# Performance work log

Measured on AMD Instinct MI355X. Metric: run time of the kernel, lower is better.

Reference implementation:

```python
import jax, jax.numpy as jnp
import numpy as np

N = 100000   # nodes
E = 800000   # edges
D_IN = 96
D_H = 96


def setup_inputs() -> dict:
    key = jax.random.key(0)
    ks = jax.random.split(key, 6)
    s = 1.0 / np.sqrt(D_IN)
    return {
        "x": jax.random.normal(ks[0], (N, D_IN), jnp.float32),
        "edge_index": jax.random.randint(ks[1], (2, E), 0, N, dtype=jnp.int32),
        "W1": jax.random.normal(ks[2], (D_IN, D_H), jnp.float32) * s,
        "b1": jnp.zeros((D_H,), jnp.float32),
        "W2": jax.random.normal(ks[3], (D_H, D_H), jnp.float32) * (1.0 / np.sqrt(D_H)),
        "b2": jnp.zeros((D_H,), jnp.float32),
    }


def _gcn_norm(edge_index, n):
    # add self-loops, then symmetric normalization deg^-1/2 * deg^-1/2 (PyG gcn_norm)
    loop = jnp.arange(n, dtype=edge_index.dtype)
    src = jnp.concatenate([edge_index[0], loop])  # [E+N] message sources
    dst = jnp.concatenate([edge_index[1], loop])  # [E+N] aggregation targets
    deg = jax.ops.segment_sum(jnp.ones_like(dst, jnp.float32), dst, num_segments=n)
    dis = jax.lax.rsqrt(deg)  # deg >= 1 thanks to self-loops
    norm = dis[src] * dis[dst]  # [E+N]
    return src, dst, norm


def _gcn_layer(x, W, b, src, dst, norm, n):
    h = x @ W                                  # [N, D] dense transform
    msg = h[src] * norm[:, None]               # [E+N, D] gather + scale
    agg = jax.ops.segment_sum(msg, dst, num_segments=n)  # scatter-add
    return agg + b


def reference(x, edge_index, W1, b1, W2, b2):
    src, dst, norm = _gcn_norm(edge_index, N)
    h = jax.nn.relu(_gcn_layer(x, W1, b1, src, dst, norm, N))
    z = jax.nn.relu(_gcn_layer(h, W2, b2, src, dst, norm, N))
    return z
```

## Files before the change

### kernel.cpp

```cpp
#include <hip/hip_runtime.h>

#define D 96
#define BSH 9
#define BNODES 512
#define MAXBUK 256


__global__ __launch_bounds__(256) void p1_hist(const int* __restrict__ ei,
                                               int* __restrict__ bcnt, int e) {
    __shared__ int h[MAXBUK];
    for (int i = threadIdx.x; i < MAXBUK; i += 256) h[i] = 0;
    __syncthreads();
    for (int i = blockIdx.x * 256 + threadIdx.x; i < e; i += gridDim.x * 256)
        atomicAdd(&h[ei[e + i] >> BSH], 1);
    __syncthreads();
    for (int i = threadIdx.x; i < MAXBUK; i += 256)
        if (h[i]) atomicAdd(&bcnt[i], h[i]);
}

__global__ void p1_scan(const int* __restrict__ bcnt, int* __restrict__ bbase,
                        int* __restrict__ bcur, int e, int nbuk) {
    __shared__ int s[MAXBUK];
    int t = threadIdx.x;
    int v = (t < nbuk) ? bcnt[t] : 0;
    s[t] = v;
    __syncthreads();
    for (int off = 1; off < MAXBUK; off <<= 1) {
        int u = (t >= off) ? s[t - off] : 0;
        __syncthreads();
        s[t] += u;
        __syncthreads();
    }
    int ex = s[t] - v;
    bbase[t] = ex;
    bcur[t] = ex;
    if (t == MAXBUK - 1) bbase[MAXBUK] = e;
}

__global__ __launch_bounds__(256) void p2_part(const int* __restrict__ ei,
                                               int* __restrict__ bcur,
                                               int2* __restrict__ pairs, int e) {
    __shared__ int h[MAXBUK];
    __shared__ int base[MAXBUK];
    __shared__ int offs[MAXBUK];
    const int CHUNK = 8192;
    int begin = blockIdx.x * CHUNK;
    int endc = min(begin + CHUNK, e);
    for (int i = threadIdx.x; i < MAXBUK; i += 256) h[i] = 0;
    __syncthreads();
    for (int i = begin + threadIdx.x; i < endc; i += 256)
        atomicAdd(&h[ei[e + i] >> BSH], 1);
    __syncthreads();
    for (int i = threadIdx.x; i < MAXBUK; i += 256) {
        int c = h[i];
        base[i] = c ? atomicAdd(&bcur[i], c) : 0;
        offs[i] = 0;
    }
    __syncthreads();
    for (int i = begin + threadIdx.x; i < endc; i += 256) {
        int d = ei[e + i], sv = ei[i];
        int b = d >> BSH;
        int r = atomicAdd(&offs[b], 1);
        pairs[base[b] + r] = make_int2(d, sv);
    }
}

__global__ __launch_bounds__(256) void p3_build(const int2* __restrict__ pairs,
                                                const int* __restrict__ bbase,
                                                int* __restrict__ rp, float* __restrict__ dis,
                                                int* __restrict__ esrc, int n, int e) {
    __shared__ int deg[BNODES];
    __shared__ int cur[BNODES];
    __shared__ int ps[256];
    int b = blockIdx.x;
    int node0 = b << BSH;
    int t = threadIdx.x;
    int pbeg = bbase[b], pend = bbase[b + 1];
    deg[t] = 0; deg[t + 256] = 0;
    __syncthreads();
    for (int i = pbeg + t; i < pend; i += 256)
        atomicAdd(&deg[pairs[i].x - node0], 1);
    __syncthreads();
    int d0 = deg[2 * t], d1 = deg[2 * t + 1];
    int pv = d0 + d1;
    ps[t] = pv;
    __syncthreads();
    for (int off = 1; off < 256; off <<= 1) {
        int u = (t >= off) ? ps[t - off] : 0;
        __syncthreads();
        ps[t] += u;
        __syncthreads();
    }
    int ex = ps[t] - pv;
    int e0 = ex, e1 = ex + d0;
    cur[2 * t] = e0; cur[2 * t + 1] = e1;
    int n0 = node0 + 2 * t, n1 = n0 + 1;
    if (n0 < n) { rp[n0] = pbeg + e0; dis[n0] = rsqrtf((float)(d0 + 1)); }
    if (n1 < n) { rp[n1] = pbeg + e1; dis[n1] = rsqrtf((float)(d1 + 1)); }
    if (b == 0 && t == 0) rp[n] = e;
    __syncthreads();
    for (int i = pbeg + t; i < pend; i += 256) {
        int2 p = pairs[i];
        int r = atomicAdd(&cur[p.x - node0], 1);
        esrc[pbeg + r] = p.y;
    }
}


__global__ void wt_kernel(const float* __restrict__ W1, const float* __restrict__ W2,
                          float* __restrict__ Wt1, float* __restrict__ Wt2) {
    int i = blockIdx.x * 256 + threadIdx.x;
    if (i < D * D) {
        int k = i / D, c = i % D;
        Wt1[c * D + k] = W1[i];
        Wt2[c * D + k] = W2[i];
    }
}


#define KC 32
#define XS_S 36
#define WT_S 36

__global__ __launch_bounds__(256) void gemm_scale(const float* __restrict__ X,
                                                  const float* __restrict__ Wt,
                                                  const float* __restrict__ dis,
                                                  float* __restrict__ out, int n) {
    __shared__ float xs[128 * XS_S];
    __shared__ float wt[96 * WT_S];
    int t = threadIdx.x;
    int row0 = blockIdx.x * 128;
    int rg = t & 15;
    int cg = t >> 4;
    float acc[8][6] = {};

    for (int kc = 0; kc < D; kc += KC) {
        for (int i = t; i < 96 * 8; i += 256) {
            int c = i >> 3, c4 = i & 7;
            float4 v = *(const float4*)&Wt[c * D + kc + c4 * 4];
            *(float4*)&wt[c * WT_S + c4 * 4] = v;
        }
        for (int i = t; i < 128 * 8; i += 256) {
            int r = i >> 3, c4 = i & 7;
            int gr = row0 + r;
            float4 v = (gr < n) ? *(const float4*)&X[(size_t)gr * D + kc + c4 * 4]
                                : make_float4(0.f, 0.f, 0.f, 0.f);
            *(float4*)&xs[r * XS_S + 4 * (c4 ^ ((r >> 3) & 7))] = v;
        }
        __syncthreads();
        #pragma unroll
        for (int k4 = 0; k4 < 8; ++k4) {
            float4 a[8], b[6];
            int xk = 4 * (k4 ^ (rg & 7));
            #pragma unroll
            for (int i = 0; i < 8; ++i)
                a[i] = *(const float4*)&xs[(rg * 8 + i) * XS_S + xk];
            #pragma unroll
            for (int j = 0; j < 6; ++j)
                b[j] = *(const float4*)&wt[(cg * 6 + j) * WT_S + k4 * 4];
            #pragma unroll
            for (int i = 0; i < 8; ++i)
                #pragma unroll
                for (int j = 0; j < 6; ++j) {
                    acc[i][j] += a[i].x * b[j].x;
                    acc[i][j] += a[i].y * b[j].y;
                    acc[i][j] += a[i].z * b[j].z;
                    acc[i][j] += a[i].w * b[j].w;
                }
        }
        __syncthreads();
    }
    #pragma unroll
    for (int i = 0; i < 8; ++i) {
        int gr = row0 + rg * 8 + i;
        if (gr < n) {
            float dsc = dis[gr];
            #pragma unroll
            for (int j = 0; j < 6; ++j)
                out[(size_t)gr * D + cg * 6 + j] = dsc * acc[i][j];
        }
    }
}


__global__ __launch_bounds__(256) void agg_kernel(const float* __restrict__ hs,
                                                  const float* __restrict__ dis,
                                                  const float* __restrict__ bias,
                                                  const int* __restrict__ rp,
                                                  const int* __restrict__ esrc,
                                                  float* __restrict__ out, int n) {
    int lane = threadIdx.x & 31;
    int node = blockIdx.x * 8 + (threadIdx.x >> 5);
    if (node >= n || lane >= 24) return;
    float4 s = ((const float4*)(hs + (size_t)node * D))[lane];
    float4 s2 = make_float4(0.f, 0.f, 0.f, 0.f);
    int beg = rp[node], end = rp[node + 1];
    int e = beg;
    for (; e + 1 < end; e += 2) {
        float4 v0 = ((const float4*)(hs + (size_t)esrc[e] * D))[lane];
        float4 v1 = ((const float4*)(hs + (size_t)esrc[e + 1] * D))[lane];
        s.x += v0.x;  s.y += v0.y;  s.z += v0.z;  s.w += v0.w;
        s2.x += v1.x; s2.y += v1.y; s2.z += v1.z; s2.w += v1.w;
    }
    if (e < end) {
        float4 v0 = ((const float4*)(hs + (size_t)esrc[e] * D))[lane];
        s.x += v0.x; s.y += v0.y; s.z += v0.z; s.w += v0.w;
    }
    float dsc = dis[node];
    float4 b = ((const float4*)bias)[lane];
    float4 o;
    o.x = fmaxf(dsc * (s.x + s2.x) + b.x, 0.f);
    o.y = fmaxf(dsc * (s.y + s2.y) + b.y, 0.f);
    o.z = fmaxf(dsc * (s.z + s2.z) + b.z, 0.f);
    o.w = fmaxf(dsc * (s.w + s2.w) + b.w, 0.f);
    ((float4*)(out + (size_t)node * D))[lane] = o;
}

extern "C" void kernel_launch(void* const* d_in, const int* in_sizes, int n_in,
                              void* d_out, int out_size, void* d_ws, size_t ws_size,
                              hipStream_t stream) {
    const float* x  = (const float*)d_in[0];
    const int*   ei = (const int*)d_in[1];
    const float* W1 = (const float*)d_in[2];
    const float* b1 = (const float*)d_in[3];
    const float* W2 = (const float*)d_in[4];
    const float* b2 = (const float*)d_in[5];
    float* out = (float*)d_out;
    int n = in_sizes[0] / D;
    int e = in_sizes[1] / 2;
    int nbuk = (n + BNODES - 1) >> BSH;

    char* ws = (char*)d_ws;
    size_t off = 0;
    auto take = [&](size_t bytes) {
        char* p = ws + off;
        off += (bytes + 511) & ~511ULL;
        return p;
    };
    int*   bcnt  = (int*)take(MAXBUK * 4);
    int*   bbase = (int*)take((MAXBUK + 1) * 4);
    int*   bcur  = (int*)take(MAXBUK * 4);
    int2*  pairs = (int2*)take((size_t)e * 8);
    int*   rp    = (int*)take((size_t)(n + 1) * 4);
    float* dsc   = (float*)take((size_t)n * 4);
    float* Wt1   = (float*)take((size_t)D * D * 4);
    float* Wt2   = (float*)take((size_t)D * D * 4);
    int*   esrc  = (int*)take((size_t)e * 4);
    float* A     = (float*)take((size_t)n * D * 4);
    float* B     = (float*)take((size_t)n * D * 4);

    hipMemsetAsync(bcnt, 0, MAXBUK * 4, stream);

    p1_hist<<<256, 256, 0, stream>>>(ei, bcnt, e);
    p1_scan<<<1, MAXBUK, 0, stream>>>(bcnt, bbase, bcur, e, nbuk);
    p2_part<<<(e + 8191) / 8192, 256, 0, stream>>>(ei, bcur, pairs, e);
    p3_build<<<nbuk, 256, 0, stream>>>(pairs, bbase, rp, dsc, esrc, n, e);
    wt_kernel<<<(2 * D * D + 255) / 256, 256, 0, stream>>>(W1, W2, Wt1, Wt2);

    int nbG = (n + 127) / 128;
    gemm_scale<<<nbG, 256, 0, stream>>>(x, Wt1, dsc, A, n);
    agg_kernel<<<(n + 7) / 8, 256, 0, stream>>>(A, dsc, b1, rp, esrc, B, n);
    gemm_scale<<<nbG, 256, 0, stream>>>(B, Wt2, dsc, A, n);
    agg_kernel<<<(n + 7) / 8, 256, 0, stream>>>(A, dsc, b2, rp, esrc, out, n);
}
```

Baseline: 325.1 us.

## Store transformed features in fp16 and use smaller CSR build buckets

The dense-transform output is now written as half precision and the aggregation kernel gathers it as half2 pairs, converting to fp32 before accumulating. This halves the bytes moved by the random neighbour gathers that dominate aggregation. Separately, the CSR build now uses 256-node buckets with twice as many of them, smaller partition chunks and more histogram blocks, for more parallelism in the preprocessing. The fp16 storage adds rounding error to the features before summation, and p1_scan now runs with 512 threads, which relies on its not-shown lines handling that block size.

```diff
diff --git a/kernel.cpp b/kernel.cpp
--- a/kernel.cpp
+++ b/kernel.cpp
@@ -1,9 +1,10 @@
 #include <hip/hip_runtime.h>
+#include <hip/hip_fp16.h>
 
 #define D 96
-#define BSH 9
-#define BNODES 512
-#define MAXBUK 256
+#define BSH 8
+#define BNODES 256
+#define MAXBUK 512
 
 
 __global__ __launch_bounds__(256) void p1_hist(const int* __restrict__ ei,
@@ -43,7 +44,7 @@
     __shared__ int h[MAXBUK];
     __shared__ int base[MAXBUK];
     __shared__ int offs[MAXBUK];
-    const int CHUNK = 8192;
+    const int CHUNK = 2048;
     int begin = blockIdx.x * CHUNK;
     int endc = min(begin + CHUNK, e);
     for (int i = threadIdx.x; i < MAXBUK; i += 256) h[i] = 0;
@@ -76,13 +77,12 @@
     int node0 = b << BSH;
     int t = threadIdx.x;
     int pbeg = bbase[b], pend = bbase[b + 1];
-    deg[t] = 0; deg[t + 256] = 0;
+    deg[t] = 0;
     __syncthreads();
     for (int i = pbeg + t; i < pend; i += 256)
         atomicAdd(&deg[pairs[i].x - node0], 1);
     __syncthreads();
-    int d0 = deg[2 * t], d1 = deg[2 * t + 1];
-    int pv = d0 + d1;
+    int pv = deg[t];
     ps[t] = pv;
     __syncthreads();
     for (int off = 1; off < 256; off <<= 1) {
@@ -92,11 +92,9 @@
         __syncthreads();
     }
     int ex = ps[t] - pv;
-    int e0 = ex, e1 = ex + d0;
-    cur[2 * t] = e0; cur[2 * t + 1] = e1;
-    int n0 = node0 + 2 * t, n1 = n0 + 1;
-    if (n0 < n) { rp[n0] = pbeg + e0; dis[n0] = rsqrtf((float)(d0 + 1)); }
-    if (n1 < n) { rp[n1] = pbeg + e1; dis[n1] = rsqrtf((float)(d1 + 1)); }
+    cur[t] = ex;
+    int n0 = node0 + t;
+    if (n0 < n) { rp[n0] = pbeg + ex; dis[n0] = rsqrtf((float)(pv + 1)); }
     if (b == 0 && t == 0) rp[n] = e;
     __syncthreads();
     for (int i = pbeg + t; i < pend; i += 256) {
@@ -125,7 +123,7 @@
 __global__ __launch_bounds__(256) void gemm_scale(const float* __restrict__ X,
                                                   const float* __restrict__ Wt,
                                                   const float* __restrict__ dis,
-                                                  float* __restrict__ out, int n) {
+                                                  __half* __restrict__ out, int n) {
     __shared__ float xs[128 * XS_S];
     __shared__ float wt[96 * WT_S];
     int t = threadIdx.x;
@@ -177,13 +175,13 @@
             float dsc = dis[gr];
             #pragma unroll
             for (int j = 0; j < 6; ++j)
-                out[(size_t)gr * D + cg * 6 + j] = dsc * acc[i][j];
-        }
-    }
-}
-
-
-__global__ __launch_bounds__(256) void agg_kernel(const float* __restrict__ hs,
+                out[(size_t)gr * D + cg * 6 + j] = __float2half(dsc * acc[i][j]);
+        }
+    }
+}
+
+
+__global__ __launch_bounds__(256) void agg_kernel(const __half* __restrict__ hs,
                                                   const float* __restrict__ dis,
                                                   const float* __restrict__ bias,
                                                   const int* __restrict__ rp,
@@ -192,27 +190,36 @@
     int lane = threadIdx.x & 31;
     int node = blockIdx.x * 8 + (threadIdx.x >> 5);
     if (node >= n || lane >= 24) return;
-    float4 s = ((const float4*)(hs + (size_t)node * D))[lane];
-    float4 s2 = make_float4(0.f, 0.f, 0.f, 0.f);
+    float2 raw = ((const float2*)(hs + (size_t)node * D))[lane];
+    __half2* hp = (__half2*)&raw;
+    float2 l0 = __half22float2(hp[0]), l1 = __half22float2(hp[1]);
+    float s0 = l0.x, s1 = l0.y, s2 = l1.x, s3 = l1.y;
+    float t0 = 0.f, t1 = 0.f, t2 = 0.f, t3 = 0.f;
     int beg = rp[node], end = rp[node + 1];
     int e = beg;
     for (; e + 1 < end; e += 2) {
-        float4 v0 = ((const float4*)(hs + (size_t)esrc[e] * D))[lane];
-        float4 v1 = ((const float4*)(hs + (size_t)esrc[e + 1] * D))[lane];
-        s.x += v0.x;  s.y += v0.y;  s.z += v0.z;  s.w += v0.w;
-        s2.x += v1.x; s2.y += v1.y; s2.z += v1.z; s2.w += v1.w;
+        float2 r0 = ((const float2*)(hs + (size_t)esrc[e] * D))[lane];
+        float2 r1 = ((const float2*)(hs + (size_t)esrc[e + 1] * D))[lane];
+        __half2* h0 = (__half2*)&r0;
+        __half2* h1 = (__half2*)&r1;
+        float2 a0 = __half22float2(h0[0]), a1 = __half22float2(h0[1]);
+        float2 b0 = __half22float2(h1[0]), b1 = __half22float2(h1[1]);
+        s0 += a0.x; s1 += a0.y; s2 += a1.x; s3 += a1.y;
+        t0 += b0.x; t1 += b0.y; t2 += b1.x; t3 += b1.y;
     }
     if (e < end) {
-        float4 v0 = ((const float4*)(hs + (size_t)esrc[e] * D))[lane];
-        s.x += v0.x; s.y += v0.y; s.z += v0.z; s.w += v0.w;
+        float2 r0 = ((const float2*)(hs + (size_t)esrc[e] * D))[lane];
+        __half2* h0 = (__half2*)&r0;
+        float2 a0 = __half22float2(h0[0]), a1 = __half22float2(h0[1]);
+        s0 += a0.x; s1 += a0.y; s2 += a1.x; s3 += a1.y;
     }
     float dsc = dis[node];
     float4 b = ((const float4*)bias)[lane];
     float4 o;
-    o.x = fmaxf(dsc * (s.x + s2.x) + b.x, 0.f);
-    o.y = fmaxf(dsc * (s.y + s2.y) + b.y, 0.f);
-    o.z = fmaxf(dsc * (s.z + s2.z) + b.z, 0.f);
-    o.w = fmaxf(dsc * (s.w + s2.w) + b.w, 0.f);
+    o.x = fmaxf(dsc * (s0 + t0) + b.x, 0.f);
+    o.y = fmaxf(dsc * (s1 + t1) + b.y, 0.f);
+    o.z = fmaxf(dsc * (s2 + t2) + b.z, 0.f);
+    o.w = fmaxf(dsc * (s3 + t3) + b.w, 0.f);
     ((float4*)(out + (size_t)node * D))[lane] = o;
 }
 
@@ -237,23 +244,23 @@
         off += (bytes + 511) & ~511ULL;
         return p;
     };
-    int*   bcnt  = (int*)take(MAXBUK * 4);
-    int*   bbase = (int*)take((MAXBUK + 1) * 4);
-    int*   bcur  = (int*)take(MAXBUK * 4);
-    int2*  pairs = (int2*)take((size_t)e * 8);
-    int*   rp    = (int*)take((size_t)(n + 1) * 4);
-    float* dsc   = (float*)take((size_t)n * 4);
-    float* Wt1   = (float*)take((size_t)D * D * 4);
-    float* Wt2   = (float*)take((size_t)D * D * 4);
-    int*   esrc  = (int*)take((size_t)e * 4);
-    float* A     = (float*)take((size_t)n * D * 4);
-    float* B     = (float*)take((size_t)n * D * 4);
+    int*    bcnt  = (int*)take(MAXBUK * 4);
+    int*    bbase = (int*)take((MAXBUK + 1) * 4);
+    int*    bcur  = (int*)take(MAXBUK * 4);
+    int2*   pairs = (int2*)take((size_t)e * 8);
+    int*    rp    = (int*)take((size_t)(n + 1) * 4);
+    float*  dsc   = (float*)take((size_t)n * 4);
+    float*  Wt1   = (float*)take((size_t)D * D * 4);
+    float*  Wt2   = (float*)take((size_t)D * D * 4);
+    int*    esrc  = (int*)take((size_t)e * 4);
+    __half* A     = (__half*)take((size_t)n * D * 2);
+    float*  B     = (float*)take((size_t)n * D * 4);
 
     hipMemsetAsync(bcnt, 0, MAXBUK * 4, stream);
 
-    p1_hist<<<256, 256, 0, stream>>>(ei, bcnt, e);
+    p1_hist<<<512, 256, 0, stream>>>(ei, bcnt, e);
     p1_scan<<<1, MAXBUK, 0, stream>>>(bcnt, bbase, bcur, e, nbuk);
-    p2_part<<<(e + 8191) / 8192, 256, 0, stream>>>(ei, bcur, pairs, e);
+    p2_part<<<(e + 2047) / 2048, 256, 0, stream>>>(ei, bcur, pairs, e);
     p3_build<<<nbuk, 256, 0, stream>>>(pairs, bbase, rp, dsc, esrc, n, e);
     wt_kernel<<<(2 * D * D + 255) / 256, 256, 0, stream>>>(W1, W2, Wt1, Wt2);
 
```

After: 300.3 us. -7.6%, faster.
